# Performance work log

Measured on AMD Instinct MI355X. Metric: run time of the kernel, lower is better.

The kernel has to match this reference:

```python
import jax, jax.numpy as jnp
import numpy as np

NUM_FEAT = 10
GAMMA = 1.0
HIDDEN = 30


def setup_inputs() -> dict:
    key = jax.random.key(0)
    ks = jax.random.split(key, 10)
    B, T = 2048, 512
    atom_i = jax.random.randint(ks[0], (B, T), 0, 118, dtype=jnp.int32)
    atom_j = jax.random.randint(ks[1], (B, T), 0, 118, dtype=jnp.int32)
    dist = jax.random.uniform(ks[2], (B, T), minval=0.5, maxval=7.0, dtype=jnp.float32)
    emb = jax.random.normal(ks[3], (118, NUM_FEAT), dtype=jnp.float32)
    s = 1.0 / np.sqrt(HIDDEN)
    W_ih = jax.random.uniform(ks[4], (3 * HIDDEN, NUM_FEAT), minval=-s, maxval=s, dtype=jnp.float32)
    W_hh = jax.random.uniform(ks[5], (3 * HIDDEN, HIDDEN), minval=-s, maxval=s, dtype=jnp.float32)
    b_ih = jax.random.uniform(ks[6], (3 * HIDDEN,), minval=-s, maxval=s, dtype=jnp.float32)
    b_hh = jax.random.uniform(ks[7], (3 * HIDDEN,), minval=-s, maxval=s, dtype=jnp.float32)
    W_out = jax.random.uniform(ks[8], (1, HIDDEN), minval=-s, maxval=s, dtype=jnp.float32)
    b_out = jax.random.uniform(ks[9], (1,), minval=-s, maxval=s, dtype=jnp.float32)
    return dict(atom_i=atom_i, atom_j=atom_j, dist=dist, emb=emb,
                W_ih=W_ih, W_hh=W_hh, b_ih=b_ih, b_hh=b_hh,
                W_out=W_out, b_out=b_out)


def _forward(atom_i, atom_j, dist, emb, W_ih, W_hh, b_ih, b_hh, W_out, b_out):
    B = atom_i.shape[0]
    mask_i = (atom_i != 0)[..., None]  # [B,T,1]
    mask_j = (atom_j != 0)[..., None]
    # conditional embedding gather: index 0 means 'no atom' -> zero vector
    e_i = jnp.where(mask_i, emb[atom_i], 0.0)  # [B,T,10]
    e_j = jnp.where(mask_j, emb[atom_j], 0.0)
    # RBF distance expansion, zeroed where atom_i is absent
    centers = jnp.arange(1, NUM_FEAT + 1, dtype=dist.dtype) * 0.7  # [10]
    rbf = jnp.exp(-GAMMA * (centers - dist[..., None]) ** 2)  # [B,T,10]
    rbf = jnp.where(mask_i, rbf, 0.0)
    feat = jnp.concatenate([e_i, e_j, rbf], axis=-1)  # [B,T,30]
    # view(B,10,-1).permute(0,2,1): row-major reshape then transpose -> [B, 3T, 10]
    x = feat.reshape(B, NUM_FEAT, -1).transpose(0, 2, 1)
    # GRU (batch_first, 1 layer); precompute input projections for all steps
    gi = jnp.einsum('bsd,hd->bsh', x, W_ih) + b_ih  # [B, 3T, 90]

    def step(h, g):
        gh = h @ W_hh.T + b_hh  # [B,90]
        i_r, i_z, i_n = jnp.split(g, 3, axis=-1)
        h_r, h_z, h_n = jnp.split(gh, 3, axis=-1)
        r = jax.nn.sigmoid(i_r + h_r)
        z = jax.nn.sigmoid(i_z + h_z)
        n = jnp.tanh(i_n + r * h_n)
        h = (1.0 - z) * n + z * h
        return h, None

    h0 = jnp.zeros((B, HIDDEN), dtype=x.dtype)
    h_last, _ = jax.lax.scan(step, h0, gi.transpose(1, 0, 2))  # only last step is used
    # dropout is identity in eval mode
    out = jax.nn.relu(h_last @ W_out.T + b_out)  # [B,1]
    return out.squeeze(-1)  # [B]


def reference(atom_i, atom_j, dist, emb, W_ih, W_hh, b_ih, b_hh, W_out, b_out):
    return _forward(atom_i, atom_j, dist, emb, W_ih, W_hh, b_ih, b_hh, W_out, b_out)
```

## Files before the change

### kernel.cpp

```cpp
#include <hip/hip_runtime.h>

#define BATCH 2048
#define T 512
#define NF 10
#define HID 30
#define S3T 1536
#define FEAT_PER_B 15360

typedef _Float16 v2h __attribute__((ext_vector_type(2)));

#define LOG2E 1.44269504088896f

__device__ __forceinline__ float fexp(float x) {
    return __builtin_amdgcn_exp2f(x * LOG2E);
}
__device__ __forceinline__ float frcp(float x) {
    return __builtin_amdgcn_rcpf(x);
}


__global__ void __launch_bounds__(512)
feat_kernel(const int* __restrict__ atom_i,
            const int* __restrict__ atom_j,
            const float* __restrict__ dist,
            const float* __restrict__ emb,
            uint4* __restrict__ xpair8) {
    __shared__ float lf[512 * 31 + 30];
    const int b = blockIdx.x;
    const int t = threadIdx.x;

    {
        const int bt = b * T + t;
        const int ai = atom_i[bt];
        const int aj = atom_j[bt];
        const float dd = dist[bt];
        const float mi = (ai != 0) ? 1.0f : 0.0f;
        const float mj = (aj != 0) ? 1.0f : 0.0f;
        const float* ei = &emb[ai * NF];
        const float* ej = &emb[aj * NF];
        float* row = &lf[t * 31];
#pragma unroll
        for (int c = 0; c < NF; ++c) row[c] = mi * ei[c];
#pragma unroll
        for (int c = 0; c < NF; ++c) row[10 + c] = mj * ej[c];
#pragma unroll
        for (int c = 0; c < NF; ++c) {
            float ctr = (float)(c + 1) * 0.7f;
            float df = ctr - dd;
            row[20 + c] = mi * fexp(-df * df);
        }
    }
    __syncthreads();

    uint4* ob = xpair8 + (long)b * 1920;
    for (int o = t; o < 1920; o += 512) {
        unsigned p  = (unsigned)o / 384u;
        unsigned c4 = (unsigned)o - p * 384u;
        union { _Float16 h[8]; uint4 u; } pk;
#pragma unroll
        for (int kx = 0; kx < 8; ++kx) {
            unsigned s = 4u * c4 + (unsigned)(kx >> 1);
            unsigned e = (unsigned)(kx & 1);
            unsigned f = (2u * p + e) * 1536u + s;
            unsigned tt = f / 30u;
            unsigned cc = f - tt * 30u;
            pk.h[kx] = (_Float16)lf[tt * 31u + cc];
        }
        ob[o] = pk.u;
    }
}

#define STEP(PAR, XQ, IDX)                                                   \
    {                                                                        \
        const uint4* hv = (const uint4*)&hbuf16[PAR][half * 32];             \
        uint4 t0 = hv[0], t1 = hv[1], t2 = hv[2], t3 = hv[3];                \
        v2h hj[16];                                                          \
        __builtin_memcpy(&hj[0], &t0, 16);                                   \
        __builtin_memcpy(&hj[4], &t1, 16);                                   \
        __builtin_memcpy(&hj[8], &t2, 16);                                   \
        __builtin_memcpy(&hj[12], &t3, 16);                                  \
        v2h xc[5];                                                           \
        _Pragma("unroll")                                                    \
        for (int pp = 0; pp < 5; ++pp) {                                     \
            unsigned w = ((const unsigned*)&XQ[pp])[IDX];                    \
            __builtin_memcpy(&xc[pp], &w, 4);                                \
        }                                                                    \
        float ar = brf, az = bzf, ai = bif, ah = bhf;                        \
        _Pragma("unroll")                                                    \
        for (int j = 0; j < 15; ++j) {                                       \
            ar = __builtin_amdgcn_fdot2(whr[j], hj[j], ar, false);           \
            az = __builtin_amdgcn_fdot2(whz[j], hj[j], az, false);           \
            ah = __builtin_amdgcn_fdot2(whn[j], hj[j], ah, false);           \
        }                                                                    \
        _Pragma("unroll")                                                    \
        for (int d = 0; d < 5; ++d) {                                        \
            ar = __builtin_amdgcn_fdot2(wir[d], xc[d], ar, false);           \
            az = __builtin_amdgcn_fdot2(wiz[d], xc[d], az, false);           \
            ai = __builtin_amdgcn_fdot2(win[d], xc[d], ai, false);           \
        }                                                                    \
        float er = __builtin_amdgcn_exp2f(ar);                               \
        float ez = __builtin_amdgcn_exp2f(az);                               \
        float rg = frcp(1.0f + er);                                          \
        float zg = frcp(1.0f + ez);                                          \
        float ng =                                                           \
            2.0f * frcp(1.0f + __builtin_amdgcn_exp2f(ai + rg * ah)) - 1.0f; \
        h = ng + zg * (h - ng);                                              \
        hbuf16[(PAR) ^ 1][half * 32 + k] = (_Float16)h;                      \
        __builtin_amdgcn_fence(__ATOMIC_ACQ_REL, "wavefront");               \
    }

__attribute__((amdgpu_waves_per_eu(1, 1)))
__global__ void __launch_bounds__(64)
gru_kernel(const _Float16* __restrict__ xpair,
           const float* __restrict__ W_ih,
           const float* __restrict__ W_hh,
           const float* __restrict__ b_ih,
           const float* __restrict__ b_hh,
           const float* __restrict__ W_out,
           const float* __restrict__ b_out,
           float* __restrict__ out) {
    __shared__ __align__(16) _Float16 hbuf16[2][64];
    const int lane = threadIdx.x;
    const int half = lane >> 5;
    const int k    = lane & 31;
    const bool active = (k < HID);
    const int kk = active ? k : (HID - 1);
    const int b = blockIdx.x * 2 + half;

    const float SRZ = -LOG2E;
    const float SN  = -2.0f * LOG2E;

    v2h whr[15], whz[15], whn[15];
    {
        const float2* Rr = (const float2*)&W_hh[(0 * HID + kk) * HID];
        const float2* Rz = (const float2*)&W_hh[(1 * HID + kk) * HID];
        const float2* Rn = (const float2*)&W_hh[(2 * HID + kk) * HID];
#pragma unroll
        for (int j = 0; j < 15; ++j) {
            float2 tr = Rr[j], tz = Rz[j], tn = Rn[j];
            whr[j] = (v2h){(_Float16)(tr.x * SRZ), (_Float16)(tr.y * SRZ)};
            whz[j] = (v2h){(_Float16)(tz.x * SRZ), (_Float16)(tz.y * SRZ)};
            whn[j] = (v2h){(_Float16)(tn.x * SN),  (_Float16)(tn.y * SN)};
        }
    }
    v2h wir[5], wiz[5], win[5];
    {
        const float2* Rr = (const float2*)&W_ih[(0 * HID + kk) * NF];
        const float2* Rz = (const float2*)&W_ih[(1 * HID + kk) * NF];
        const float2* Rn = (const float2*)&W_ih[(2 * HID + kk) * NF];
#pragma unroll
        for (int d = 0; d < 5; ++d) {
            float2 tr = Rr[d], tz = Rz[d], tn = Rn[d];
            wir[d] = (v2h){(_Float16)(tr.x * SRZ), (_Float16)(tr.y * SRZ)};
            wiz[d] = (v2h){(_Float16)(tz.x * SRZ), (_Float16)(tz.y * SRZ)};
            win[d] = (v2h){(_Float16)(tn.x * SN),  (_Float16)(tn.y * SN)};
        }
    }
    const float brf = SRZ * (b_ih[0 * HID + kk] + b_hh[0 * HID + kk]);
    const float bzf = SRZ * (b_ih[1 * HID + kk] + b_hh[1 * HID + kk]);
    const float bif = SN * b_ih[2 * HID + kk];
    const float bhf = SN * b_hh[2 * HID + kk];

    const _Float16* xb = xpair + (long)b * FEAT_PER_B;
    const uint4* xa[5];
#pragma unroll
    for (int p = 0; p < 5; ++p) xa[p] = (const uint4*)(xb + p * 3072);

    hbuf16[0][lane] = (_Float16)0.0f;
    hbuf16[1][lane] = (_Float16)0.0f;
    __builtin_amdgcn_fence(__ATOMIC_ACQ_REL, "wavefront");

    float h = 0.0f;
    uint4 xq0[5], xq1[5];
#pragma unroll
    for (int p = 0; p < 5; ++p) xq0[p] = xa[p][0];

    for (int c2 = 0; c2 < 384; c2 += 2) {
#pragma unroll
        for (int p = 0; p < 5; ++p) xq1[p] = xa[p][c2 + 1];
        STEP(0, xq0, 0);
        STEP(1, xq0, 1);
        STEP(0, xq0, 2);
        STEP(1, xq0, 3);
        const int cn = (c2 + 2 < 384) ? (c2 + 2) : 383;
#pragma unroll
        for (int p = 0; p < 5; ++p) xq0[p] = xa[p][cn];
        STEP(0, xq1, 0);
        STEP(1, xq1, 1);
        STEP(0, xq1, 2);
        STEP(1, xq1, 3);
    }

    float v = active ? h * W_out[kk] : 0.0f;
#pragma unroll
    for (int off = 16; off; off >>= 1) v += __shfl_xor(v, off, 32);
    if (k == 0) {
        float o = v + b_out[0];
        out[b] = o > 0.0f ? o : 0.0f;
    }
}

extern "C" void kernel_launch(void* const* d_in, const int* in_sizes, int n_in,
                              void* d_out, int out_size, void* d_ws, size_t ws_size,
                              hipStream_t stream) {
    const int* atom_i   = (const int*)d_in[0];
    const int* atom_j   = (const int*)d_in[1];
    const float* dist   = (const float*)d_in[2];
    const float* emb    = (const float*)d_in[3];
    const float* W_ih   = (const float*)d_in[4];
    const float* W_hh   = (const float*)d_in[5];
    const float* b_ih   = (const float*)d_in[6];
    const float* b_hh   = (const float*)d_in[7];
    const float* W_out  = (const float*)d_in[8];
    const float* b_out  = (const float*)d_in[9];
    float* out = (float*)d_out;
    _Float16* xpair = (_Float16*)d_ws;

    feat_kernel<<<BATCH, 512, 0, stream>>>(atom_i, atom_j, dist, emb,
                                           (uint4*)xpair);
    gru_kernel<<<BATCH / 2, 64, 0, stream>>>(xpair, W_ih, W_hh, b_ih, b_hh,
                                             W_out, b_out, out);
}
```

Measured before the change: 389.7 us.

## Split each GRU hidden-unit dot product across wave halves with permlane32 swap

```diff
diff --git a/kernel.cpp b/kernel.cpp
--- a/kernel.cpp
+++ b/kernel.cpp
@@ -18,6 +18,12 @@
     return __builtin_amdgcn_rcpf(x);
 }
 
+__device__ __forceinline__ float half_sum(float a) {
+    unsigned ua = __builtin_bit_cast(unsigned, a);
+    auto r = __builtin_amdgcn_permlane32_swap(ua, ua, false, false);
+    return __builtin_bit_cast(float, (unsigned)r[0]) +
+           __builtin_bit_cast(float, (unsigned)r[1]);
+}
 
 __global__ void __launch_bounds__(512)
 feat_kernel(const int* __restrict__ atom_i,
@@ -72,32 +78,32 @@
 
 #define STEP(PAR, XQ, IDX)                                                   \
     {                                                                        \
-        const uint4* hv = (const uint4*)&hbuf16[PAR][half * 32];             \
-        uint4 t0 = hv[0], t1 = hv[1], t2 = hv[2], t3 = hv[3];                \
-        v2h hj[16];                                                          \
-        __builtin_memcpy(&hj[0], &t0, 16);                                   \
-        __builtin_memcpy(&hj[4], &t1, 16);                                   \
-        __builtin_memcpy(&hj[8], &t2, 16);                                   \
-        __builtin_memcpy(&hj[12], &t3, 16);                                  \
-        v2h xc[5];                                                           \
+        const uint4* hv = (const uint4*)&hbuf16[PAR][half * 48];             \
+        uint4 t0 = hv[0], t1 = hv[1];                                        \
+        v2h xc[3];                                                           \
         _Pragma("unroll")                                                    \
-        for (int pp = 0; pp < 5; ++pp) {                                     \
+        for (int pp = 0; pp < 3; ++pp) {                                     \
             unsigned w = ((const unsigned*)&XQ[pp])[IDX];                    \
             __builtin_memcpy(&xc[pp], &w, 4);                                \
         }                                                                    \
         float ar = brf, az = bzf, ai = bif, ah = bhf;                        \
         _Pragma("unroll")                                                    \
-        for (int j = 0; j < 15; ++j) {                                       \
+        for (int d = 0; d < 3; ++d) {                                        \
+            ar = __builtin_amdgcn_fdot2(wir[d], xc[d], ar, false);           \
+            az = __builtin_amdgcn_fdot2(wiz[d], xc[d], az, false);           \
+            ai = __builtin_amdgcn_fdot2(win[d], xc[d], ai, false);           \
+        }                                                                    \
+        v2h hj[8];                                                           \
+        __builtin_memcpy(&hj[0], &t0, 16);                                   \
+        __builtin_memcpy(&hj[4], &t1, 16);                                   \
+        _Pragma("unroll")                                                    \
+        for (int j = 0; j < 8; ++j) {                                        \
             ar = __builtin_amdgcn_fdot2(whr[j], hj[j], ar, false);           \
             az = __builtin_amdgcn_fdot2(whz[j], hj[j], az, false);           \
             ah = __builtin_amdgcn_fdot2(whn[j], hj[j], ah, false);           \
         }                                                                    \
-        _Pragma("unroll")                                                    \
-        for (int d = 0; d < 5; ++d) {                                        \
-            ar = __builtin_amdgcn_fdot2(wir[d], xc[d], ar, false);           \
-            az = __builtin_amdgcn_fdot2(wiz[d], xc[d], az, false);           \
-            ai = __builtin_amdgcn_fdot2(win[d], xc[d], ai, false);           \
-        }                                                                    \
+        ar = half_sum(ar); az = half_sum(az);                                \
+        ai = half_sum(ai); ah = half_sum(ah);                                \
         float er = __builtin_amdgcn_exp2f(ar);                               \
         float ez = __builtin_amdgcn_exp2f(az);                               \
         float rg = frcp(1.0f + er);                                          \
@@ -109,7 +115,7 @@
         __builtin_amdgcn_fence(__ATOMIC_ACQ_REL, "wavefront");               \
     }
 
-__attribute__((amdgpu_waves_per_eu(1, 1)))
+__attribute__((amdgpu_waves_per_eu(2, 2)))
 __global__ void __launch_bounds__(64)
 gru_kernel(const _Float16* __restrict__ xpair,
            const float* __restrict__ W_ih,
@@ -125,66 +131,79 @@
     const int k    = lane & 31;
     const bool active = (k < HID);
     const int kk = active ? k : (HID - 1);
-    const int b = blockIdx.x * 2 + half;
+    const int b = blockIdx.x;
 
     const float SRZ = -LOG2E;
     const float SN  = -2.0f * LOG2E;
 
-    v2h whr[15], whz[15], whn[15];
+    v2h whr[8], whz[8], whn[8];
     {
-        const float2* Rr = (const float2*)&W_hh[(0 * HID + kk) * HID];
-        const float2* Rz = (const float2*)&W_hh[(1 * HID + kk) * HID];
-        const float2* Rn = (const float2*)&W_hh[(2 * HID + kk) * HID];
-#pragma unroll
-        for (int j = 0; j < 15; ++j) {
-            float2 tr = Rr[j], tz = Rz[j], tn = Rn[j];
-            whr[j] = (v2h){(_Float16)(tr.x * SRZ), (_Float16)(tr.y * SRZ)};
-            whz[j] = (v2h){(_Float16)(tz.x * SRZ), (_Float16)(tz.y * SRZ)};
-            whn[j] = (v2h){(_Float16)(tn.x * SN),  (_Float16)(tn.y * SN)};
-        }
-    }
-    v2h wir[5], wiz[5], win[5];
+        const float* Rr = &W_hh[(0 * HID + kk) * HID];
+        const float* Rz = &W_hh[(1 * HID + kk) * HID];
+        const float* Rn = &W_hh[(2 * HID + kk) * HID];
+        const int jb = half * 8;
+#pragma unroll
+        for (int j = 0; j < 8; ++j) {
+            const int c  = (jb + j) * 2;
+            const int cs = (c < HID) ? c : 0;
+            const float mrz = (c < HID) ? SRZ : 0.0f;
+            const float mn  = (c < HID) ? SN  : 0.0f;
+            whr[j] = (v2h){(_Float16)(Rr[cs] * mrz), (_Float16)(Rr[cs + 1] * mrz)};
+            whz[j] = (v2h){(_Float16)(Rz[cs] * mrz), (_Float16)(Rz[cs + 1] * mrz)};
+            whn[j] = (v2h){(_Float16)(Rn[cs] * mn),  (_Float16)(Rn[cs + 1] * mn)};
+        }
+    }
+    v2h wir[3], wiz[3], win[3];
+    const int db = half * 3;
     {
-        const float2* Rr = (const float2*)&W_ih[(0 * HID + kk) * NF];
-        const float2* Rz = (const float2*)&W_ih[(1 * HID + kk) * NF];
-        const float2* Rn = (const float2*)&W_ih[(2 * HID + kk) * NF];
-#pragma unroll
-        for (int d = 0; d < 5; ++d) {
-            float2 tr = Rr[d], tz = Rz[d], tn = Rn[d];
-            wir[d] = (v2h){(_Float16)(tr.x * SRZ), (_Float16)(tr.y * SRZ)};
-            wiz[d] = (v2h){(_Float16)(tz.x * SRZ), (_Float16)(tz.y * SRZ)};
-            win[d] = (v2h){(_Float16)(tn.x * SN),  (_Float16)(tn.y * SN)};
-        }
-    }
-    const float brf = SRZ * (b_ih[0 * HID + kk] + b_hh[0 * HID + kk]);
-    const float bzf = SRZ * (b_ih[1 * HID + kk] + b_hh[1 * HID + kk]);
-    const float bif = SN * b_ih[2 * HID + kk];
-    const float bhf = SN * b_hh[2 * HID + kk];
+        const float* Rr = &W_ih[(0 * HID + kk) * NF];
+        const float* Rz = &W_ih[(1 * HID + kk) * NF];
+        const float* Rn = &W_ih[(2 * HID + kk) * NF];
+#pragma unroll
+        for (int i = 0; i < 3; ++i) {
+            const int d  = db + i;
+            const int dd = (d < 5) ? d * 2 : 0;
+            const float mrz = (d < 5) ? SRZ : 0.0f;
+            const float mn  = (d < 5) ? SN  : 0.0f;
+            wir[i] = (v2h){(_Float16)(Rr[dd] * mrz), (_Float16)(Rr[dd + 1] * mrz)};
+            wiz[i] = (v2h){(_Float16)(Rz[dd] * mrz), (_Float16)(Rz[dd + 1] * mrz)};
+            win[i] = (v2h){(_Float16)(Rn[dd] * mn),  (_Float16)(Rn[dd + 1] * mn)};
+        }
+    }
+    const float en  = (half == 0) ? 1.0f : 0.0f;
+    const float brf = en * SRZ * (b_ih[0 * HID + kk] + b_hh[0 * HID + kk]);
+    const float bzf = en * SRZ * (b_ih[1 * HID + kk] + b_hh[1 * HID + kk]);
+    const float bif = en * SN * b_ih[2 * HID + kk];
+    const float bhf = en * SN * b_hh[2 * HID + kk];
 
     const _Float16* xb = xpair + (long)b * FEAT_PER_B;
-    const uint4* xa[5];
-#pragma unroll
-    for (int p = 0; p < 5; ++p) xa[p] = (const uint4*)(xb + p * 3072);
+    const uint4* xa[3];
+#pragma unroll
+    for (int i = 0; i < 3; ++i) {
+        int s = db + i;
+        if (s > 4) s = 4;
+        xa[i] = (const uint4*)(xb + s * 3072);
+    }
 
     hbuf16[0][lane] = (_Float16)0.0f;
     hbuf16[1][lane] = (_Float16)0.0f;
     __builtin_amdgcn_fence(__ATOMIC_ACQ_REL, "wavefront");
 
     float h = 0.0f;
-    uint4 xq0[5], xq1[5];
-#pragma unroll
-    for (int p = 0; p < 5; ++p) xq0[p] = xa[p][0];
+    uint4 xq0[3], xq1[3];
+#pragma unroll
+    for (int p = 0; p < 3; ++p) xq0[p] = xa[p][0];
 
     for (int c2 = 0; c2 < 384; c2 += 2) {
 #pragma unroll
-        for (int p = 0; p < 5; ++p) xq1[p] = xa[p][c2 + 1];
+        for (int p = 0; p < 3; ++p) xq1[p] = xa[p][c2 + 1];
         STEP(0, xq0, 0);
         STEP(1, xq0, 1);
         STEP(0, xq0, 2);
         STEP(1, xq0, 3);
         const int cn = (c2 + 2 < 384) ? (c2 + 2) : 383;
 #pragma unroll
-        for (int p = 0; p < 5; ++p) xq0[p] = xa[p][cn];
+        for (int p = 0; p < 3; ++p) xq0[p] = xa[p][cn];
         STEP(0, xq1, 0);
         STEP(1, xq1, 1);
         STEP(0, xq1, 2);
@@ -194,7 +213,7 @@
     float v = active ? h * W_out[kk] : 0.0f;
 #pragma unroll
     for (int off = 16; off; off >>= 1) v += __shfl_xor(v, off, 32);
-    if (k == 0) {
+    if (lane == 0) {
         float o = v + b_out[0];
         out[b] = o > 0.0f ? o : 0.0f;
     }
@@ -218,6 +237,6 @@
 
     feat_kernel<<<BATCH, 512, 0, stream>>>(atom_i, atom_j, dist, emb,
                                            (uint4*)xpair);
-    gru_kernel<<<BATCH / 2, 64, 0, stream>>>(xpair, W_ih, W_hh, b_ih, b_hh,
-                                             W_out, b_out, out);
-}
+    gru_kernel<<<BATCH, 64, 0, stream>>>(xpair, W_ih, W_hh, b_ih, b_hh,
+                                         W_out, b_out, out);
+}
```

Measured after the change: 544.9 us. 39.8% more time.

## Broadcast GRU hidden state via DPP and permlane16_swap instead of LDS

Applied to the files above, without the earlier changes.

```diff
diff --git a/kernel.cpp b/kernel.cpp
--- a/kernel.cpp
+++ b/kernel.cpp
@@ -18,6 +18,16 @@
     return __builtin_amdgcn_rcpf(x);
 }
 
+#define DPP_QPERM_XOR1 0xB1
+#define DPP_ROR2       0x122
+#define DPP_ROR4       0x124
+#define DPP_ROR8       0x128
+
+template <int CTRL>
+__device__ __forceinline__ unsigned dppmov(unsigned v) {
+    return (unsigned)__builtin_amdgcn_update_dpp(0, (int)v, CTRL, 0xF, 0xF,
+                                                 false);
+}
 
 __global__ void __launch_bounds__(512)
 feat_kernel(const int* __restrict__ atom_i,
@@ -70,15 +80,29 @@
     }
 }
 
-#define STEP(PAR, XQ, IDX)                                                   \
+#define STEP(XQ, IDX)                                                        \
     {                                                                        \
-        const uint4* hv = (const uint4*)&hbuf16[PAR][half * 32];             \
-        uint4 t0 = hv[0], t1 = hv[1], t2 = hv[2], t3 = hv[3];                \
-        v2h hj[16];                                                          \
-        __builtin_memcpy(&hj[0], &t0, 16);                                   \
-        __builtin_memcpy(&hj[4], &t1, 16);                                   \
-        __builtin_memcpy(&hj[8], &t2, 16);                                   \
-        __builtin_memcpy(&hj[12], &t3, 16);                                  \
+        unsigned hf = (unsigned)__builtin_bit_cast(unsigned short,           \
+                                                   (_Float16)h);             \
+        unsigned nb = dppmov<DPP_QPERM_XOR1>(hf);                            \
+        unsigned gg0 = hf | (nb << 16);                                      \
+        unsigned gg1 = dppmov<DPP_ROR2>(gg0);                                \
+        unsigned gg2 = dppmov<DPP_ROR4>(gg0);                                \
+        unsigned gg3 = dppmov<DPP_ROR4>(gg1);                                \
+        unsigned gg4 = dppmov<DPP_ROR8>(gg0);                                \
+        unsigned gg5 = dppmov<DPP_ROR8>(gg1);                                \
+        unsigned gg6 = dppmov<DPP_ROR8>(gg2);                                \
+        unsigned gg7 = dppmov<DPP_ROR8>(gg3);                                \
+        unsigned gg[8] = {gg0, gg1, gg2, gg3, gg4, gg5, gg6, gg7};           \
+        v2h hp[16];                                                          \
+        _Pragma("unroll")                                                    \
+        for (int i = 0; i < 8; ++i) {                                        \
+            auto rr = __builtin_amdgcn_permlane16_swap((unsigned)gg[i],      \
+                                                       (unsigned)gg[i],      \
+                                                       false, false);        \
+            hp[i]     = __builtin_bit_cast(v2h, (unsigned)rr[0]);            \
+            hp[8 + i] = __builtin_bit_cast(v2h, (unsigned)rr[1]);            \
+        }                                                                    \
         v2h xc[5];                                                           \
         _Pragma("unroll")                                                    \
         for (int pp = 0; pp < 5; ++pp) {                                     \
@@ -86,17 +110,17 @@
             __builtin_memcpy(&xc[pp], &w, 4);                                \
         }                                                                    \
         float ar = brf, az = bzf, ai = bif, ah = bhf;                        \
-        _Pragma("unroll")                                                    \
-        for (int j = 0; j < 15; ++j) {                                       \
-            ar = __builtin_amdgcn_fdot2(whr[j], hj[j], ar, false);           \
-            az = __builtin_amdgcn_fdot2(whz[j], hj[j], az, false);           \
-            ah = __builtin_amdgcn_fdot2(whn[j], hj[j], ah, false);           \
-        }                                                                    \
         _Pragma("unroll")                                                    \
         for (int d = 0; d < 5; ++d) {                                        \
             ar = __builtin_amdgcn_fdot2(wir[d], xc[d], ar, false);           \
             az = __builtin_amdgcn_fdot2(wiz[d], xc[d], az, false);           \
             ai = __builtin_amdgcn_fdot2(win[d], xc[d], ai, false);           \
+        }                                                                    \
+        _Pragma("unroll")                                                    \
+        for (int j = 0; j < 16; ++j) {                                       \
+            ar = __builtin_amdgcn_fdot2(whr[j], hp[j], ar, false);           \
+            az = __builtin_amdgcn_fdot2(whz[j], hp[j], az, false);           \
+            ah = __builtin_amdgcn_fdot2(whn[j], hp[j], ah, false);           \
         }                                                                    \
         float er = __builtin_amdgcn_exp2f(ar);                               \
         float ez = __builtin_amdgcn_exp2f(az);                               \
@@ -105,8 +129,6 @@
         float ng =                                                           \
             2.0f * frcp(1.0f + __builtin_amdgcn_exp2f(ai + rg * ah)) - 1.0f; \
         h = ng + zg * (h - ng);                                              \
-        hbuf16[(PAR) ^ 1][half * 32 + k] = (_Float16)h;                      \
-        __builtin_amdgcn_fence(__ATOMIC_ACQ_REL, "wavefront");               \
     }
 
 __attribute__((amdgpu_waves_per_eu(1, 1)))
@@ -119,7 +141,6 @@
            const float* __restrict__ W_out,
            const float* __restrict__ b_out,
            float* __restrict__ out) {
-    __shared__ __align__(16) _Float16 hbuf16[2][64];
     const int lane = threadIdx.x;
     const int half = lane >> 5;
     const int k    = lane & 31;
@@ -130,17 +151,53 @@
     const float SRZ = -LOG2E;
     const float SN  = -2.0f * LOG2E;
 
-    v2h whr[15], whz[15], whn[15];
-    {
-        const float2* Rr = (const float2*)&W_hh[(0 * HID + kk) * HID];
-        const float2* Rz = (const float2*)&W_hh[(1 * HID + kk) * HID];
-        const float2* Rn = (const float2*)&W_hh[(2 * HID + kk) * HID];
-#pragma unroll
-        for (int j = 0; j < 15; ++j) {
-            float2 tr = Rr[j], tz = Rz[j], tn = Rn[j];
-            whr[j] = (v2h){(_Float16)(tr.x * SRZ), (_Float16)(tr.y * SRZ)};
-            whz[j] = (v2h){(_Float16)(tz.x * SRZ), (_Float16)(tz.y * SRZ)};
-            whn[j] = (v2h){(_Float16)(tn.x * SN),  (_Float16)(tn.y * SN)};
+    int pidx[16];
+    {
+        int p0 = (lane & 31) >> 1;
+        unsigned q0 = (unsigned)p0;
+        unsigned q1 = dppmov<DPP_ROR2>(q0);
+        unsigned q2 = dppmov<DPP_ROR4>(q0);
+        unsigned q3 = dppmov<DPP_ROR4>(q1);
+        unsigned q4 = dppmov<DPP_ROR8>(q0);
+        unsigned q5 = dppmov<DPP_ROR8>(q1);
+        unsigned q6 = dppmov<DPP_ROR8>(q2);
+        unsigned q7 = dppmov<DPP_ROR8>(q3);
+        unsigned qs[8] = {q0, q1, q2, q3, q4, q5, q6, q7};
+#pragma unroll
+        for (int i = 0; i < 8; ++i) {
+            auto rr = __builtin_amdgcn_permlane16_swap((unsigned)qs[i],
+                                                       (unsigned)qs[i],
+                                                       false, false);
+            pidx[i]     = (int)rr[0];
+            pidx[8 + i] = (int)rr[1];
+        }
+    }
+
+    v2h whr[16], whz[16], whn[16];
+    {
+        const float* Rr = &W_hh[(0 * HID + kk) * HID];
+        const float* Rz = &W_hh[(1 * HID + kk) * HID];
+        const float* Rn = &W_hh[(2 * HID + kk) * HID];
+        const bool odd = (lane & 1) != 0;
+#pragma unroll
+        for (int i = 0; i < 16; ++i) {
+            const int p = pidx[i];
+            const bool real = (p < 15);
+            const int c = real ? 2 * p : 0;
+            const float srz = real ? SRZ : 0.0f;
+            const float sn  = real ? SN  : 0.0f;
+            float r0 = Rr[c] * srz, r1 = Rr[c + 1] * srz;
+            float z0 = Rz[c] * srz, z1 = Rz[c + 1] * srz;
+            float n0 = Rn[c] * sn,  n1 = Rn[c + 1] * sn;
+            if (odd) {
+                float tt;
+                tt = r0; r0 = r1; r1 = tt;
+                tt = z0; z0 = z1; z1 = tt;
+                tt = n0; n0 = n1; n1 = tt;
+            }
+            whr[i] = (v2h){(_Float16)r0, (_Float16)r1};
+            whz[i] = (v2h){(_Float16)z0, (_Float16)z1};
+            whn[i] = (v2h){(_Float16)n0, (_Float16)n1};
         }
     }
     v2h wir[5], wiz[5], win[5];
@@ -166,10 +223,6 @@
 #pragma unroll
     for (int p = 0; p < 5; ++p) xa[p] = (const uint4*)(xb + p * 3072);
 
-    hbuf16[0][lane] = (_Float16)0.0f;
-    hbuf16[1][lane] = (_Float16)0.0f;
-    __builtin_amdgcn_fence(__ATOMIC_ACQ_REL, "wavefront");
-
     float h = 0.0f;
     uint4 xq0[5], xq1[5];
 #pragma unroll
@@ -178,17 +231,17 @@
     for (int c2 = 0; c2 < 384; c2 += 2) {
 #pragma unroll
         for (int p = 0; p < 5; ++p) xq1[p] = xa[p][c2 + 1];
-        STEP(0, xq0, 0);
-        STEP(1, xq0, 1);
-        STEP(0, xq0, 2);
-        STEP(1, xq0, 3);
+        STEP(xq0, 0);
+        STEP(xq0, 1);
+        STEP(xq0, 2);
+        STEP(xq0, 3);
         const int cn = (c2 + 2 < 384) ? (c2 + 2) : 383;
 #pragma unroll
         for (int p = 0; p < 5; ++p) xq0[p] = xa[p][cn];
-        STEP(0, xq1, 0);
-        STEP(1, xq1, 1);
-        STEP(0, xq1, 2);
-        STEP(1, xq1, 3);
+        STEP(xq1, 0);
+        STEP(xq1, 1);
+        STEP(xq1, 2);
+        STEP(xq1, 3);
     }
 
     float v = active ? h * W_out[kk] : 0.0f;
```

Result: slower. 469.6 us (+20.5%).

## Interleave two batch recurrences per wave and split dot-product accumulators

Applied to the files above, without the earlier changes.

```diff
diff --git a/kernel.cpp b/kernel.cpp
--- a/kernel.cpp
+++ b/kernel.cpp
@@ -16,6 +16,9 @@
 }
 __device__ __forceinline__ float frcp(float x) {
     return __builtin_amdgcn_rcpf(x);
+}
+__device__ __forceinline__ float fd(v2h a, v2h b, float c) {
+    return __builtin_amdgcn_fdot2(a, b, c, false);
 }
 
 
@@ -70,42 +73,105 @@
     }
 }
 
-#define STEP(PAR, XQ, IDX)                                                   \
+#define STEP2(PAR, XQA, XQB, IDX)                                            \
     {                                                                        \
-        const uint4* hv = (const uint4*)&hbuf16[PAR][half * 32];             \
-        uint4 t0 = hv[0], t1 = hv[1], t2 = hv[2], t3 = hv[3];                \
-        v2h hj[16];                                                          \
-        __builtin_memcpy(&hj[0], &t0, 16);                                   \
-        __builtin_memcpy(&hj[4], &t1, 16);                                   \
-        __builtin_memcpy(&hj[8], &t2, 16);                                   \
-        __builtin_memcpy(&hj[12], &t3, 16);                                  \
-        v2h xc[5];                                                           \
+        const uint4* hvA = (const uint4*)&hbufA[PAR][half * 32];             \
+        uint4 ta0 = hvA[0], ta1 = hvA[1], ta2 = hvA[2], ta3 = hvA[3];        \
+        const uint4* hvB = (const uint4*)&hbufB[PAR][half * 32];             \
+        uint4 tb0 = hvB[0], tb1 = hvB[1], tb2 = hvB[2], tb3 = hvB[3];        \
+        v2h xcA[5], xcB[5];                                                  \
         _Pragma("unroll")                                                    \
         for (int pp = 0; pp < 5; ++pp) {                                     \
-            unsigned w = ((const unsigned*)&XQ[pp])[IDX];                    \
-            __builtin_memcpy(&xc[pp], &w, 4);                                \
-        }                                                                    \
-        float ar = brf, az = bzf, ai = bif, ah = bhf;                        \
-        _Pragma("unroll")                                                    \
-        for (int j = 0; j < 15; ++j) {                                       \
-            ar = __builtin_amdgcn_fdot2(whr[j], hj[j], ar, false);           \
-            az = __builtin_amdgcn_fdot2(whz[j], hj[j], az, false);           \
-            ah = __builtin_amdgcn_fdot2(whn[j], hj[j], ah, false);           \
-        }                                                                    \
+            unsigned wa = ((const unsigned*)&XQA[pp])[IDX];                  \
+            __builtin_memcpy(&xcA[pp], &wa, 4);                              \
+            unsigned wb = ((const unsigned*)&XQB[pp])[IDX];                  \
+            __builtin_memcpy(&xcB[pp], &wb, 4);                              \
+        }                                                                    \
+        float arA0 = brf, azA0 = bzf, aiA = bif, ahA0 = bhf;                 \
+        float arB0 = brf, azB0 = bzf, aiB = bif, ahB0 = bhf;                 \
         _Pragma("unroll")                                                    \
         for (int d = 0; d < 5; ++d) {                                        \
-            ar = __builtin_amdgcn_fdot2(wir[d], xc[d], ar, false);           \
-            az = __builtin_amdgcn_fdot2(wiz[d], xc[d], az, false);           \
-            ai = __builtin_amdgcn_fdot2(win[d], xc[d], ai, false);           \
-        }                                                                    \
-        float er = __builtin_amdgcn_exp2f(ar);                               \
-        float ez = __builtin_amdgcn_exp2f(az);                               \
-        float rg = frcp(1.0f + er);                                          \
-        float zg = frcp(1.0f + ez);                                          \
-        float ng =                                                           \
-            2.0f * frcp(1.0f + __builtin_amdgcn_exp2f(ai + rg * ah)) - 1.0f; \
-        h = ng + zg * (h - ng);                                              \
-        hbuf16[(PAR) ^ 1][half * 32 + k] = (_Float16)h;                      \
+            arA0 = fd(wir[d], xcA[d], arA0);                                 \
+            azA0 = fd(wiz[d], xcA[d], azA0);                                 \
+            aiA  = fd(win[d], xcA[d], aiA);                                  \
+            arB0 = fd(wir[d], xcB[d], arB0);                                 \
+            azB0 = fd(wiz[d], xcB[d], azB0);                                 \
+            aiB  = fd(win[d], xcB[d], aiB);                                  \
+        }                                                                    \
+        v2h hjA[16];                                                         \
+        __builtin_memcpy(&hjA[0], &ta0, 16);                                 \
+        __builtin_memcpy(&hjA[4], &ta1, 16);                                 \
+        __builtin_memcpy(&hjA[8], &ta2, 16);                                 \
+        __builtin_memcpy(&hjA[12], &ta3, 16);                                \
+        float arA1 = 0.0f, arA2 = 0.0f, arA3 = 0.0f;                         \
+        float azA1 = 0.0f, azA2 = 0.0f, azA3 = 0.0f;                         \
+        float ahA1 = 0.0f, ahA2 = 0.0f;                                      \
+        _Pragma("unroll")                                                    \
+        for (int j = 0; j < 5; ++j) {                                        \
+            arA1 = fd(whr[j], hjA[j], arA1);                                 \
+            azA1 = fd(whz[j], hjA[j], azA1);                                 \
+            ahA0 = fd(whn[j], hjA[j], ahA0);                                 \
+        }                                                                    \
+        _Pragma("unroll")                                                    \
+        for (int j = 5; j < 10; ++j) {                                       \
+            arA2 = fd(whr[j], hjA[j], arA2);                                 \
+            azA2 = fd(whz[j], hjA[j], azA2);                                 \
+            ahA1 = fd(whn[j], hjA[j], ahA1);                                 \
+        }                                                                    \
+        _Pragma("unroll")                                                    \
+        for (int j = 10; j < 15; ++j) {                                      \
+            arA3 = fd(whr[j], hjA[j], arA3);                                 \
+            azA3 = fd(whz[j], hjA[j], azA3);                                 \
+            ahA2 = fd(whn[j], hjA[j], ahA2);                                 \
+        }                                                                    \
+        v2h hjB[16];                                                         \
+        __builtin_memcpy(&hjB[0], &tb0, 16);                                 \
+        __builtin_memcpy(&hjB[4], &tb1, 16);                                 \
+        __builtin_memcpy(&hjB[8], &tb2, 16);                                 \
+        __builtin_memcpy(&hjB[12], &tb3, 16);                                \
+        float arB1 = 0.0f, arB2 = 0.0f, arB3 = 0.0f;                         \
+        float azB1 = 0.0f, azB2 = 0.0f, azB3 = 0.0f;                         \
+        float ahB1 = 0.0f, ahB2 = 0.0f;                                      \
+        _Pragma("unroll")                                                    \
+        for (int j = 0; j < 5; ++j) {                                        \
+            arB1 = fd(whr[j], hjB[j], arB1);                                 \
+            azB1 = fd(whz[j], hjB[j], azB1);                                 \
+            ahB0 = fd(whn[j], hjB[j], ahB0);                                 \
+        }                                                                    \
+        _Pragma("unroll")                                                    \
+        for (int j = 5; j < 10; ++j) {                                       \
+            arB2 = fd(whr[j], hjB[j], arB2);                                 \
+            azB2 = fd(whz[j], hjB[j], azB2);                                 \
+            ahB1 = fd(whn[j], hjB[j], ahB1);                                 \
+        }                                                                    \
+        _Pragma("unroll")                                                    \
+        for (int j = 10; j < 15; ++j) {                                      \
+            arB3 = fd(whr[j], hjB[j], arB3);                                 \
+            azB3 = fd(whz[j], hjB[j], azB3);                                 \
+            ahB2 = fd(whn[j], hjB[j], ahB2);                                 \
+        }                                                                    \
+        float arA = (arA0 + arA1) + (arA2 + arA3);                           \
+        float azA = (azA0 + azA1) + (azA2 + azA3);                           \
+        float ahA = (ahA0 + ahA1) + ahA2;                                    \
+        float erA = __builtin_amdgcn_exp2f(arA);                             \
+        float ezA = __builtin_amdgcn_exp2f(azA);                             \
+        float arB = (arB0 + arB1) + (arB2 + arB3);                           \
+        float azB = (azB0 + azB1) + (azB2 + azB3);                           \
+        float ahB = (ahB0 + ahB1) + ahB2;                                    \
+        float erB = __builtin_amdgcn_exp2f(arB);                             \
+        float ezB = __builtin_amdgcn_exp2f(azB);                             \
+        float rgA = frcp(1.0f + erA);                                        \
+        float zgA = frcp(1.0f + ezA);                                        \
+        float rgB = frcp(1.0f + erB);                                        \
+        float zgB = frcp(1.0f + ezB);                                        \
+        float ngA = 2.0f * frcp(1.0f +                                       \
+                    __builtin_amdgcn_exp2f(aiA + rgA * ahA)) - 1.0f;         \
+        float ngB = 2.0f * frcp(1.0f +                                       \
+                    __builtin_amdgcn_exp2f(aiB + rgB * ahB)) - 1.0f;         \
+        hA = ngA + zgA * (hA - ngA);                                         \
+        hB = ngB + zgB * (hB - ngB);                                         \
+        hbufA[(PAR) ^ 1][half * 32 + k] = (_Float16)hA;                      \
+        hbufB[(PAR) ^ 1][half * 32 + k] = (_Float16)hB;                      \
         __builtin_amdgcn_fence(__ATOMIC_ACQ_REL, "wavefront");               \
     }
 
@@ -119,13 +185,15 @@
            const float* __restrict__ W_out,
            const float* __restrict__ b_out,
            float* __restrict__ out) {
-    __shared__ __align__(16) _Float16 hbuf16[2][64];
+    __shared__ __align__(16) _Float16 hbufA[2][64];
+    __shared__ __align__(16) _Float16 hbufB[2][64];
     const int lane = threadIdx.x;
     const int half = lane >> 5;
     const int k    = lane & 31;
     const bool active = (k < HID);
     const int kk = active ? k : (HID - 1);
-    const int b = blockIdx.x * 2 + half;
+    const int bA = blockIdx.x * 4 + half;
+    const int bB = bA + 2;
 
     const float SRZ = -LOG2E;
     const float SN  = -2.0f * LOG2E;
@@ -161,42 +229,69 @@
     const float bif = SN * b_ih[2 * HID + kk];
     const float bhf = SN * b_hh[2 * HID + kk];
 
-    const _Float16* xb = xpair + (long)b * FEAT_PER_B;
-    const uint4* xa[5];
-#pragma unroll
-    for (int p = 0; p < 5; ++p) xa[p] = (const uint4*)(xb + p * 3072);
-
-    hbuf16[0][lane] = (_Float16)0.0f;
-    hbuf16[1][lane] = (_Float16)0.0f;
+    const _Float16* xbA = xpair + (long)bA * FEAT_PER_B;
+    const _Float16* xbB = xpair + (long)bB * FEAT_PER_B;
+    const uint4* xaA[5];
+    const uint4* xaB[5];
+#pragma unroll
+    for (int p = 0; p < 5; ++p) {
+        xaA[p] = (const uint4*)(xbA + p * 3072);
+        xaB[p] = (const uint4*)(xbB + p * 3072);
+    }
+
+    hbufA[0][lane] = (_Float16)0.0f;
+    hbufA[1][lane] = (_Float16)0.0f;
+    hbufB[0][lane] = (_Float16)0.0f;
+    hbufB[1][lane] = (_Float16)0.0f;
     __builtin_amdgcn_fence(__ATOMIC_ACQ_REL, "wavefront");
 
-    float h = 0.0f;
-    uint4 xq0[5], xq1[5];
-#pragma unroll
-    for (int p = 0; p < 5; ++p) xq0[p] = xa[p][0];
+    float hA = 0.0f, hB = 0.0f;
+    uint4 xqA0[5], xqA1[5], xqB0[5], xqB1[5];
+#pragma unroll
+    for (int p = 0; p < 5; ++p) {
+        xqA0[p] = xaA[p][0];
+        xqB0[p] = xaB[p][0];
+    }
 
     for (int c2 = 0; c2 < 384; c2 += 2) {
 #pragma unroll
-        for (int p = 0; p < 5; ++p) xq1[p] = xa[p][c2 + 1];
-        STEP(0, xq0, 0);
-        STEP(1, xq0, 1);
-        STEP(0, xq0, 2);
-        STEP(1, xq0, 3);
+        for (int p = 0; p < 5; ++p) {
+            xqA1[p] = xaA[p][c2 + 1];
+            xqB1[p] = xaB[p][c2 + 1];
+        }
+        STEP2(0, xqA0, xqB0, 0);
+        STEP2(1, xqA0, xqB0, 1);
+        STEP2(0, xqA0, xqB0, 2);
+        STEP2(1, xqA0, xqB0, 3);
         const int cn = (c2 + 2 < 384) ? (c2 + 2) : 383;
 #pragma unroll
-        for (int p = 0; p < 5; ++p) xq0[p] = xa[p][cn];
-        STEP(0, xq1, 0);
-        STEP(1, xq1, 1);
-        STEP(0, xq1, 2);
-        STEP(1, xq1, 3);
-    }
-
-    float v = active ? h * W_out[kk] : 0.0f;
-#pragma unroll
-    for (int off = 16; off; off >>= 1) v += __shfl_xor(v, off, 32);
-    if (k == 0) {
-        float o = v + b_out[0];
-        out[b] = o > 0.0f ? o : 0.0f;
+        for (int p = 0; p < 5; ++p) {
+            xqA0[p] = xaA[p][cn];
+            xqB0[p] = xaB[p][cn];
+        }
+        STEP2(0, xqA1, xqB1, 0);
+        STEP2(1, xqA1, xqB1, 1);
+        STEP2(0, xqA1, xqB1, 2);
+        STEP2(1, xqA1, xqB1, 3);
+    }
+
+    {
+        float v = active ? hA * W_out[kk] : 0.0f;
+#pragma unroll
+        for (int off = 16; off; off >>= 1) v += __shfl_xor(v, off, 32);
+        if (k == 0) {
+            float o = v + b_out[0];
+            out[bA] = o > 0.0f ? o : 0.0f;
+        }
+    }
+    {
+        float v = active ? hB * W_out[kk] : 0.0f;
+#pragma unroll
+        for (int off = 16; off; off >>= 1) v += __shfl_xor(v, off, 32);
+        if (k == 0) {
+            float o = v + b_out[0];
+            out[bB] = o > 0.0f ? o : 0.0f;
+        }
     }
 }
 
@@ -218,6 +313,6 @@
 
     feat_kernel<<<BATCH, 512, 0, stream>>>(atom_i, atom_j, dist, emb,
                                            (uint4*)xpair);
-    gru_kernel<<<BATCH / 2, 64, 0, stream>>>(xpair, W_ih, W_hh, b_ih, b_hh,
+    gru_kernel<<<BATCH / 4, 64, 0, stream>>>(xpair, W_ih, W_hh, b_ih, b_hh,
                                              W_out, b_out, out);
 }
```

New measurement: 725.6 us. +86.2%, slower.
